# Kernel tuning notes

Hardware: AMD Instinct MI355X
Metric: run time of the kernel (lower is better)

The kernel has to match this reference:

```python
import jax, jax.numpy as jnp
import numpy as np

B, NPTS, T, P, C, D = 2, 32768, 32768, 512, 4, 768


def _sincos_pos_embed(centers, embed_dim):
    # centers: np [P,3]; matches get_3d_sincos_pos_embed
    c = centers - centers.mean(axis=0)
    c = c / np.linalg.norm(c, axis=1).max()
    div = np.exp(np.arange(0, embed_dim, 6) * -(np.log(10000.0) / embed_dim))  # [D/6]
    arg = c[:, None, :] * div[None, :, None]                                   # [P, D/6, 3]
    pe = np.concatenate([np.sin(arg), np.cos(arg)], axis=-1).reshape(centers.shape[0], embed_dim)
    return pe.astype(np.float32)


def setup_inputs() -> dict:
    key = jax.random.key(0)
    ks = jax.random.split(key, 12)
    rng = np.random.default_rng(0)

    # ragged patch sizes (avg 64) summing exactly to T
    sizes = rng.integers(32, 97, size=P).astype(np.int64)
    sizes = np.maximum((sizes * (T / sizes.sum())).astype(np.int64), 1)
    sizes[-1] += T - sizes.sum()
    patch_offset = jnp.asarray(np.concatenate([[0], np.cumsum(sizes)]), dtype=jnp.int32)  # [P+1]

    patch_index = jax.random.randint(ks[0], (T,), 0, NPTS, dtype=jnp.int32)
    latent = jax.random.normal(ks[1], (B, NPTS, C), dtype=jnp.float32)

    s = 0.02
    params = dict(
        w1a=jax.random.normal(ks[2], (C, D), jnp.float32) * s,
        b1a=jnp.zeros((D,), jnp.float32),
        w1b=jax.random.normal(ks[3], (D, D), jnp.float32) * s,
        b1b=jnp.zeros((D,), jnp.float32),
        w2a=jax.random.normal(ks[4], (2 * D, D), jnp.float32) * s,
        b2a=jnp.zeros((D,), jnp.float32),
        g2=jnp.ones((D,), jnp.float32),
        beta2=jnp.zeros((D,), jnp.float32),
        w2b=jax.random.normal(ks[5], (D, D), jnp.float32) * s,
        b2b=jnp.zeros((D,), jnp.float32),
    )

    centers = rng.standard_normal((P, 3))
    pos_embed = jnp.asarray(_sincos_pos_embed(centers, D))[None]  # [1, P, D]

    return dict(latent=latent, patch_index=patch_index, patch_offset=patch_offset,
                pos_embed=pos_embed, **params)


def _ln(x, eps, gamma=None, beta=None):
    mu = x.mean(axis=-1, keepdims=True)
    var = ((x - mu) ** 2).mean(axis=-1, keepdims=True)
    y = (x - mu) * jax.lax.rsqrt(var + eps)
    if gamma is not None:
        y = y * gamma + beta
    return y


def reference(latent, patch_index, patch_offset, pos_embed,
              w1a, b1a, w1b, b1b, w2a, b2a, g2, beta2, w2b, b2b):
    T_ = patch_index.shape[0]
    P_ = patch_offset.shape[0] - 1
    # segment id of each token (repeat_interleave inverse): seg[t] = patch containing t
    seg = jnp.searchsorted(patch_offset[1:], jnp.arange(T_, dtype=patch_offset.dtype), side='right')

    x = latent[:, patch_index, :]                           # [B, T, C] gather
    h = x @ w1a + b1a
    h = jax.nn.gelu(_ln(h, 1e-6), approximate=False)
    h = h @ w1b + b1b                                       # [B, T, D]

    segmax = lambda a: jax.ops.segment_max(a, seg, num_segments=P_)
    y = jax.vmap(segmax)(h)                                 # [B, P, D] ragged max-pool

    h2 = jnp.concatenate([y[:, seg, :], h], axis=-1)        # repeat_interleave + concat
    h2 = h2 @ w2a + b2a
    h2 = jax.nn.gelu(_ln(h2, 1e-5, g2, beta2), approximate=False)
    h2 = h2 @ w2b + b2b                                     # [B, T, D]
    raw_latent = h2

    out = jax.vmap(segmax)(raw_latent) + pos_embed          # [B, P, D]
    return out.astype(raw_latent.dtype), raw_latent
```

## Files before the change

kernel.cpp:

```cpp
#include <hip/hip_runtime.h>
#include <hip/hip_bf16.h>
#include <math.h>

#define B_    2
#define NPTS_ 32768
#define T_    32768
#define P_    512
#define C_    4
#define D_    768
#define M_    (B_ * T_)

typedef __bf16 bf16_t;
typedef __bf16 bf16x8 __attribute__((ext_vector_type(8)));
typedef __bf16 bf16x4 __attribute__((ext_vector_type(4)));
typedef float  f32x4  __attribute__((ext_vector_type(4)));

__device__ inline void gload16(const void* g, void* l) {
  __builtin_amdgcn_global_load_lds(
      (const __attribute__((address_space(1))) void*)g,
      (__attribute__((address_space(3))) void*)l, 16, 0, 0);
}

__device__ inline float gelu_exact(float x) {
  return 0.5f * x * (1.0f + erff(x * 0.70710678118654752f));
}

__device__ inline unsigned fmap(float x) {
  unsigned u = __float_as_uint(x);
  return (u & 0x80000000u) ? ~u : (u | 0x80000000u);
}
__device__ inline float funmap(unsigned u) {
  unsigned v = (u & 0x80000000u) ? (u & 0x7FFFFFFFu) : ~u;
  return __uint_as_float(v);
}

__global__ void seg_kernel(const int* __restrict__ off, int* __restrict__ seg) {
  int t = blockIdx.x * blockDim.x + threadIdx.x;
  if (t >= T_) return;
  int lo = 0, hi = P_;
  while (lo < hi) {
    int mid = (lo + hi) >> 1;
    if (off[mid + 1] <= t) lo = mid + 1; else hi = mid;
  }
  seg[t] = lo;
}

__global__ __launch_bounds__(256) void init_umax_kernel(uint4* __restrict__ u) {
  u[blockIdx.x * 256 + threadIdx.x] = make_uint4(0, 0, 0, 0);
}

__global__ __launch_bounds__(256) void yconv_kernel(
    const uint4* __restrict__ ymax, bf16_t* __restrict__ y) {
  int t = blockIdx.x * 256 + threadIdx.x;
  uint4 u = ymax[t];
  bf16x4 o;
  o[0] = (bf16_t)funmap(u.x); o[1] = (bf16_t)funmap(u.y);
  o[2] = (bf16_t)funmap(u.z); o[3] = (bf16_t)funmap(u.w);
  *(bf16x4*)(y + (size_t)t * 4) = o;
}

__global__ __launch_bounds__(256) void final2_kernel(
    const uint4* __restrict__ rmax, const float4* __restrict__ pe,
    float4* __restrict__ out) {
  int t = blockIdx.x * 256 + threadIdx.x;
  int row = t / 192, col = t % 192;
  uint4 u = rmax[t];
  float4 p = pe[(row & (P_ - 1)) * 192 + col];
  float4 o;
  o.x = funmap(u.x) + p.x; o.y = funmap(u.y) + p.y;
  o.z = funmap(u.z) + p.z; o.w = funmap(u.w) + p.w;
  out[t] = o;
}

__global__ __launch_bounds__(256) void wconvT_kernel(
    const float* __restrict__ src, bf16_t* __restrict__ dst, int K, int N) {
  __shared__ float tile[32][33];
  int n0 = blockIdx.x * 32, k0 = blockIdx.y * 32;
  int tx = threadIdx.x, ty = threadIdx.y;
  #pragma unroll
  for (int i = 0; i < 4; ++i)
    tile[ty + 8 * i][tx] = src[(size_t)(k0 + ty + 8 * i) * N + n0 + tx];
  __syncthreads();
  #pragma unroll
  for (int i = 0; i < 4; ++i)
    dst[(size_t)(n0 + ty + 8 * i) * K + k0 + tx] = (bf16_t)tile[tx][ty + 8 * i];
}

__global__ __launch_bounds__(256) void embed_kernel(
    const float4* __restrict__ latent4, const int* __restrict__ pidx,
    const float* __restrict__ w1a, const float* __restrict__ b1a,
    bf16_t* __restrict__ act1) {
  int wid = threadIdx.x >> 6, lane = threadIdx.x & 63;
  int m = blockIdx.x * 4 + wid;
  int b = m >> 15, t = m & (T_ - 1);
  float4 x = latent4[(size_t)b * NPTS_ + pidx[t]];
  int d8 = lane * 8, d4 = 512 + lane * 4;
  float v[12];
  {
    float4 a0 = *(const float4*)(b1a + d8);
    float4 a1 = *(const float4*)(b1a + d8 + 4);
    float4 a2 = *(const float4*)(b1a + d4);
    v[0]=a0.x; v[1]=a0.y; v[2]=a0.z; v[3]=a0.w;
    v[4]=a1.x; v[5]=a1.y; v[6]=a1.z; v[7]=a1.w;
    v[8]=a2.x; v[9]=a2.y; v[10]=a2.z; v[11]=a2.w;
  }
  float xk[4] = {x.x, x.y, x.z, x.w};
  #pragma unroll
  for (int k = 0; k < 4; ++k) {
    const float* w = w1a + k * D_;
    float4 w0 = *(const float4*)(w + d8);
    float4 w1 = *(const float4*)(w + d8 + 4);
    float4 w2 = *(const float4*)(w + d4);
    float f = xk[k];
    v[0] += f*w0.x; v[1] += f*w0.y; v[2] += f*w0.z; v[3] += f*w0.w;
    v[4] += f*w1.x; v[5] += f*w1.y; v[6] += f*w1.z; v[7] += f*w1.w;
    v[8] += f*w2.x; v[9] += f*w2.y; v[10]+= f*w2.z; v[11]+= f*w2.w;
  }
  float sum = 0.f, sq = 0.f;
  #pragma unroll
  for (int j = 0; j < 12; ++j) { sum += v[j]; sq += v[j]*v[j]; }
  #pragma unroll
  for (int o = 32; o > 0; o >>= 1) { sum += __shfl_xor(sum, o); sq += __shfl_xor(sq, o); }
  float mu = sum * (1.0f / D_);
  float rstd = rsqrtf(sq * (1.0f / D_) - mu * mu + 1e-6f);
  bf16x8 o8; bf16x4 o4;
  #pragma unroll
  for (int j = 0; j < 8; ++j) o8[j] = (bf16_t)gelu_exact((v[j] - mu) * rstd);
  #pragma unroll
  for (int j = 0; j < 4; ++j) o4[j] = (bf16_t)gelu_exact((v[8 + j] - mu) * rstd);
  size_t base = (size_t)m * D_;
  *(bf16x8*)(act1 + base + d8) = o8;
  *(bf16x4*)(act1 + base + d4) = o4;
}

__global__ __launch_bounds__(256) void ln2_kernel(
    const bf16_t* __restrict__ h2pre, const float* __restrict__ z,
    const int* __restrict__ seg, const float* __restrict__ g2,
    const float* __restrict__ beta2, bf16_t* __restrict__ act2) {
  int wid = threadIdx.x >> 6, lane = threadIdx.x & 63;
  int m = blockIdx.x * 4 + wid;
  int b = m >> 15, t = m & (T_ - 1);
  int d8 = lane * 8, d4 = 512 + lane * 4;
  size_t base = (size_t)m * D_;
  const float* zrow = z + (size_t)((b << 9) + seg[t]) * D_;
  bf16x8 i8 = *(const bf16x8*)(h2pre + base + d8);
  bf16x4 i4 = *(const bf16x4*)(h2pre + base + d4);
  float4 z0 = *(const float4*)(zrow + d8);
  float4 z1 = *(const float4*)(zrow + d8 + 4);
  float4 z2 = *(const float4*)(zrow + d4);
  float v[12];
  #pragma unroll
  for (int j = 0; j < 8; ++j) v[j] = (float)i8[j];
  #pragma unroll
  for (int j = 0; j < 4; ++j) v[8 + j] = (float)i4[j];
  v[0]+=z0.x; v[1]+=z0.y; v[2]+=z0.z; v[3]+=z0.w;
  v[4]+=z1.x; v[5]+=z1.y; v[6]+=z1.z; v[7]+=z1.w;
  v[8]+=z2.x; v[9]+=z2.y; v[10]+=z2.z; v[11]+=z2.w;
  float sum = 0.f, sq = 0.f;
  #pragma unroll
  for (int j = 0; j < 12; ++j) { sum += v[j]; sq += v[j]*v[j]; }
  #pragma unroll
  for (int o = 32; o > 0; o >>= 1) { sum += __shfl_xor(sum, o); sq += __shfl_xor(sq, o); }
  float mu = sum * (1.0f / D_);
  float rstd = rsqrtf(sq * (1.0f / D_) - mu * mu + 1e-5f);
  float4 ga = *(const float4*)(g2 + d8);
  float4 gb = *(const float4*)(g2 + d8 + 4);
  float4 gc = *(const float4*)(g2 + d4);
  float4 ba = *(const float4*)(beta2 + d8);
  float4 bb = *(const float4*)(beta2 + d8 + 4);
  float4 bc = *(const float4*)(beta2 + d4);
  float g[12] = {ga.x,ga.y,ga.z,ga.w, gb.x,gb.y,gb.z,gb.w, gc.x,gc.y,gc.z,gc.w};
  float be[12]= {ba.x,ba.y,ba.z,ba.w, bb.x,bb.y,bb.z,bb.w, bc.x,bc.y,bc.z,bc.w};
  bf16x8 o8; bf16x4 o4;
  #pragma unroll
  for (int j = 0; j < 8; ++j) o8[j] = (bf16_t)gelu_exact((v[j] - mu) * rstd * g[j] + be[j]);
  #pragma unroll
  for (int j = 0; j < 4; ++j) o4[j] = (bf16_t)gelu_exact((v[8+j] - mu) * rstd * g[8+j] + be[8+j]);
  *(bf16x8*)(act2 + base + d8) = o8;
  *(bf16x4*)(act2 + base + d4) = o4;
}

template <int MODE, bool SEGMAX, typename OutT>
__global__ __launch_bounds__(256) void gemm_kernel(
    const bf16_t* __restrict__ A, const bf16_t* __restrict__ BT,
    const float* __restrict__ addend, OutT* __restrict__ C,
    int M, int N, int K, const int* __restrict__ seg,
    unsigned* __restrict__ gmax) {
  __shared__ bf16_t As[128 * 32];
  __shared__ bf16_t Bs[128 * 32];
  __shared__ int segm[128];
  int tid = threadIdx.x;
  int wave = tid >> 6, lane = tid & 63;
  int lr = lane & 15, hi = lane >> 4;
  int wm = wave >> 1, wn = wave & 1;

  int nb = gridDim.x * gridDim.y;
  int bid = blockIdx.y * gridDim.x + blockIdx.x;
  int per = nb >> 3;
  int w = (bid & 7) * per + (bid >> 3);
  int wx = w % gridDim.x, wy = w / gridDim.x;
  int n0 = wx * 128, m0 = wy * 128;

  if (SEGMAX) {
    if (tid < 128) segm[tid] = seg[(m0 + tid) & (T_ - 1)];
  }

  f32x4 acc[4][4] = {};

  for (int kt = 0; kt < K; kt += 32) {
    __syncthreads();
    #pragma unroll
    for (int q = 0; q < 2; ++q) {
      int c = q * 256 + tid;
      int row = c >> 2, ko = (c & 3) * 8;
      gload16(A + (size_t)(m0 + row) * K + (kt + ko), (char*)As + q * 4096 + wave * 1024);
      gload16(BT + (size_t)(n0 + row) * K + (kt + ko), (char*)Bs + q * 4096 + wave * 1024);
    }
    __syncthreads();

    bf16x8 af[4], bfr[4];
    #pragma unroll
    for (int i = 0; i < 4; ++i)
      af[i] = *reinterpret_cast<const bf16x8*>(&As[(size_t)(wm * 64 + i * 16 + lr) * 32 + hi * 8]);
    #pragma unroll
    for (int j = 0; j < 4; ++j)
      bfr[j] = *reinterpret_cast<const bf16x8*>(&Bs[(size_t)(wn * 64 + j * 16 + lr) * 32 + hi * 8]);
    #pragma unroll
    for (int i = 0; i < 4; ++i)
      #pragma unroll
      for (int j = 0; j < 4; ++j)
        acc[i][j] = __builtin_amdgcn_mfma_f32_16x16x32_bf16(af[i], bfr[j], acc[i][j], 0, 0, 0);
  }

  unsigned* smax = reinterpret_cast<unsigned*>(As);
  int sb = 0, zb = 0;
  if (SEGMAX) {
    __syncthreads();
    for (int q = tid; q < 8 * 128; q += 256) smax[q] = 0u;
    sb = segm[0];
    zb = (m0 >> 15) << 9;
    __syncthreads();
  }

  #pragma unroll
  for (int j = 0; j < 4; ++j) {
    int nl = wn * 64 + j * 16 + lr;
    int n = n0 + nl;
    float bv = (MODE == 0) ? addend[n] : 0.f;
    #pragma unroll
    for (int i = 0; i < 4; ++i) {
      int rbase = wm * 64 + i * 16 + hi * 4;
      float vv[4];
      #pragma unroll
      for (int r = 0; r < 4; ++r) {
        vv[r] = acc[i][j][r] + bv;
        C[(size_t)(m0 + rbase + r) * N + n] = (OutT)vv[r];
      }
      if (SEGMAX) {
        int sA = segm[rbase] - sb, sB = segm[rbase + 3] - sb;
        if (sA == sB) {
          float mx = fmaxf(fmaxf(vv[0], vv[1]), fmaxf(vv[2], vv[3]));
          atomicMax(&smax[sA * 128 + nl], fmap(mx));
        } else {
          #pragma unroll
          for (int r = 0; r < 4; ++r)
            atomicMax(&smax[(segm[rbase + r] - sb) * 128 + nl], fmap(vv[r]));
        }
      }
    }
  }

  if (SEGMAX) {
    __syncthreads();
    int nseg = segm[127] - sb + 1;
    for (int q = tid; q < nseg * 128; q += 256) {
      int sl = q >> 7, nl2 = q & 127;
      atomicMax(&gmax[(size_t)(zb + sb + sl) * D_ + n0 + nl2], smax[q]);
    }
  }
}

extern "C" void kernel_launch(void* const* d_in, const int* in_sizes, int n_in,
                              void* d_out, int out_size, void* d_ws, size_t ws_size,
                              hipStream_t stream) {
  const float* latent       = (const float*)d_in[0];
  const int*   patch_index  = (const int*)d_in[1];
  const int*   patch_offset = (const int*)d_in[2];
  const float* pos_embed    = (const float*)d_in[3];
  const float* w1a  = (const float*)d_in[4];
  const float* b1a  = (const float*)d_in[5];
  const float* w1b  = (const float*)d_in[6];
  const float* b1b  = (const float*)d_in[7];
  const float* w2a  = (const float*)d_in[8];
  const float* b2a  = (const float*)d_in[9];
  const float* g2   = (const float*)d_in[10];
  const float* beta2= (const float*)d_in[11];
  const float* w2b  = (const float*)d_in[12];
  const float* b2b  = (const float*)d_in[13];

  float* out_f   = (float*)d_out;
  float* raw_out = out_f + (size_t)B_ * P_ * D_;

  char* ws = (char*)d_ws;
  size_t off = 0;
  auto take = [&](size_t bytes) {
    off = (off + 255) & ~(size_t)255;
    char* p = ws + off;
    off += bytes;
    return p;
  };
  int*      seg   = (int*)     take((size_t)T_ * 4);
  bf16_t*   w1bT  = (bf16_t*)  take((size_t)D_ * D_ * 2);
  bf16_t*   w2aTT = (bf16_t*)  take((size_t)D_ * D_ * 2);
  bf16_t*   w2aBT = (bf16_t*)  take((size_t)D_ * D_ * 2);
  bf16_t*   w2bT  = (bf16_t*)  take((size_t)D_ * D_ * 2);
  bf16_t*   ybuf  = (bf16_t*)  take((size_t)B_ * P_ * D_ * 2);
  float*    zbuf  = (float*)   take((size_t)B_ * P_ * D_ * 4);
  unsigned* umax  = (unsigned*)take((size_t)2 * B_ * P_ * D_ * 4);
  unsigned* ymax  = umax;
  unsigned* rmax  = umax + (size_t)B_ * P_ * D_;
  bf16_t*   bufY  = (bf16_t*)  take((size_t)M_ * D_ * 2);
  size_t needX = (size_t)M_ * D_ * 2;
  size_t offX  = (off + 255) & ~(size_t)255;
  bf16_t* bufX;
  if (offX + needX <= ws_size) {
    bufX = (bf16_t*)take(needX);
  } else {
    bufX = (bf16_t*)raw_out;
  }

  seg_kernel<<<(T_ + 255) / 256, 256, 0, stream>>>(patch_offset, seg);
  init_umax_kernel<<<(2 * B_ * P_ * D_) / (4 * 256), 256, 0, stream>>>((uint4*)umax);
  dim3 wcb(32, 8);
  wconvT_kernel<<<dim3(D_/32, D_/32), wcb, 0, stream>>>(w1b, w1bT, D_, D_);
  wconvT_kernel<<<dim3(D_/32, D_/32), wcb, 0, stream>>>(w2a, w2aTT, D_, D_);
  wconvT_kernel<<<dim3(D_/32, D_/32), wcb, 0, stream>>>(w2a + (size_t)D_*D_, w2aBT, D_, D_);
  wconvT_kernel<<<dim3(D_/32, D_/32), wcb, 0, stream>>>(w2b, w2bT, D_, D_);

  embed_kernel<<<M_ / 4, 256, 0, stream>>>((const float4*)latent, patch_index, w1a, b1a, bufX);

  gemm_kernel<0, true, bf16_t><<<dim3(D_/128, M_/128), 256, 0, stream>>>(
      bufX, w1bT, b1b, bufY, M_, D_, D_, seg, ymax);

  yconv_kernel<<<(B_ * P_ * D_) / (4 * 256), 256, 0, stream>>>((const uint4*)ymax, ybuf);

  gemm_kernel<0, false, float><<<dim3(D_/128, (B_*P_)/128), 256, 0, stream>>>(
      ybuf, w2aTT, b2a, zbuf, B_*P_, D_, D_, nullptr, nullptr);

  gemm_kernel<1, false, bf16_t><<<dim3(D_/128, M_/128), 256, 0, stream>>>(
      bufY, w2aBT, nullptr, bufX, M_, D_, D_, nullptr, nullptr);

  ln2_kernel<<<M_ / 4, 256, 0, stream>>>(bufX, zbuf, seg, g2, beta2, bufY);

  gemm_kernel<0, true, float><<<dim3(D_/128, M_/128), 256, 0, stream>>>(
      bufY, w2bT, b2b, raw_out, M_, D_, D_, seg, rmax);

  final2_kernel<<<(B_ * P_ * D_) / (4 * 256), 256, 0, stream>>>(
      (const uint4*)rmax, (const float4*)pos_embed, (float4*)out_f);
}
```

Measured before the change: 535.5 us.

## Replace 128x128 GEMM with double-buffered 256x256 tile kernel using swizzled LDS

Replaces the simple 128x128, K=32 single-buffered GEMM with a 256x256-tile, 512-thread kernel. It uses K=64 steps, two LDS stages (128KB) filled by async global-to-LDS loads, and an XOR-swizzled LDS layout to avoid bank conflicts. The main loop interleaves fragment loads, prefetch of the next stage and MFMA bursts with setprio and barriers, aiming to hide memory latency and raise MFMA utilisation. The small GEMM over 1024 rows now launches only 12 blocks, and the large LDS footprint limits each CU to one block.

Result: faster. 456.9 us (-14.7%).

```diff
diff --git a/kernel.cpp b/kernel.cpp
--- a/kernel.cpp
+++ b/kernel.cpp
@@ -180,91 +180,182 @@
   *(bf16x4*)(act2 + base + d4) = o4;
 }
 
-template <int MODE, bool SEGMAX, typename OutT>
-__global__ __launch_bounds__(256) void gemm_kernel(
+#define STAGE_A(P2, KTG)                                                     \
+  { _Pragma("unroll")                                                        \
+    for (int h = 0; h < 2; ++h) {                                            \
+      _Pragma("unroll")                                                      \
+      for (int ps = 0; ps < 2; ++ps) {                                       \
+        int c = ps * 512 + wid * 64 + lane;                                  \
+        int rw = c >> 3;                                                     \
+        int cs = (c & 7) ^ (rw & 7);                                         \
+        gload16(A + (size_t)(m0 + h * 128 + rw) * 768 + (KTG) + cs * 8,      \
+                lds + (P2) * 65536 + h * 16384 + ps * 8192 + wid * 1024);    \
+      } } }
+
+#define STAGE_B(P2, KTG)                                                     \
+  { _Pragma("unroll")                                                        \
+    for (int h = 0; h < 2; ++h) {                                            \
+      _Pragma("unroll")                                                      \
+      for (int ps = 0; ps < 2; ++ps) {                                       \
+        int c = ps * 512 + wid * 64 + lane;                                  \
+        int rw = c >> 3;                                                     \
+        int cs = (c & 7) ^ (rw & 7);                                         \
+        gload16(BT + (size_t)(n0 + h * 128 + rw) * 768 + (KTG) + cs * 8,     \
+                lds + (P2) * 65536 + 32768 + h * 16384 + ps * 8192 + wid * 1024); \
+      } } }
+
+template <bool HASBIAS, bool SEGMAX, typename OutT>
+__global__ __launch_bounds__(512, 1) void gemm256_kernel(
     const bf16_t* __restrict__ A, const bf16_t* __restrict__ BT,
-    const float* __restrict__ addend, OutT* __restrict__ C,
-    int M, int N, int K, const int* __restrict__ seg,
-    unsigned* __restrict__ gmax) {
-  __shared__ bf16_t As[128 * 32];
-  __shared__ bf16_t Bs[128 * 32];
-  __shared__ int segm[128];
+    const float* __restrict__ bias, OutT* __restrict__ C,
+    const int* __restrict__ seg, unsigned* __restrict__ gmax) {
+  constexpr int NT = 12;
+  __shared__ __align__(16) char lds[131072];
+  __shared__ int segm[256];
   int tid = threadIdx.x;
-  int wave = tid >> 6, lane = tid & 63;
+  int wid = tid >> 6, lane = tid & 63;
   int lr = lane & 15, hi = lane >> 4;
-  int wm = wave >> 1, wn = wave & 1;
-
-  int nb = gridDim.x * gridDim.y;
-  int bid = blockIdx.y * gridDim.x + blockIdx.x;
-  int per = nb >> 3;
-  int w = (bid & 7) * per + (bid >> 3);
-  int wx = w % gridDim.x, wy = w / gridDim.x;
-  int n0 = wx * 128, m0 = wy * 128;
-
-  if (SEGMAX) {
-    if (tid < 128) segm[tid] = seg[(m0 + tid) & (T_ - 1)];
-  }
-
-  f32x4 acc[4][4] = {};
-
-  for (int kt = 0; kt < K; kt += 32) {
-    __syncthreads();
-    #pragma unroll
-    for (int q = 0; q < 2; ++q) {
-      int c = q * 256 + tid;
-      int row = c >> 2, ko = (c & 3) * 8;
-      gload16(A + (size_t)(m0 + row) * K + (kt + ko), (char*)As + q * 4096 + wave * 1024);
-      gload16(BT + (size_t)(n0 + row) * K + (kt + ko), (char*)Bs + q * 4096 + wave * 1024);
-    }
-    __syncthreads();
-
-    bf16x8 af[4], bfr[4];
-    #pragma unroll
-    for (int i = 0; i < 4; ++i)
-      af[i] = *reinterpret_cast<const bf16x8*>(&As[(size_t)(wm * 64 + i * 16 + lr) * 32 + hi * 8]);
-    #pragma unroll
-    for (int j = 0; j < 4; ++j)
-      bfr[j] = *reinterpret_cast<const bf16x8*>(&Bs[(size_t)(wn * 64 + j * 16 + lr) * 32 + hi * 8]);
-    #pragma unroll
-    for (int i = 0; i < 4; ++i)
-      #pragma unroll
-      for (int j = 0; j < 4; ++j)
-        acc[i][j] = __builtin_amdgcn_mfma_f32_16x16x32_bf16(af[i], bfr[j], acc[i][j], 0, 0, 0);
-  }
-
-  unsigned* smax = reinterpret_cast<unsigned*>(As);
+  int wm = wid >> 2, wn = wid & 3;
+
+  int gx = gridDim.x;
+  int nb = gx * gridDim.y;
+  int bid = blockIdx.y * gx + blockIdx.x;
+  int w = ((nb & 7) == 0) ? ((bid & 7) * (nb >> 3) + (bid >> 3)) : bid;
+  int bx = w % gx, by = w / gx;
+  int n0 = bx * 256, m0 = by * 256;
+
+  if (SEGMAX) { if (tid < 256) segm[tid] = seg[(m0 + tid) & (T_ - 1)]; }
+
+  f32x4 acc[8][4] = {};
+  bf16x8 af0[4][2], af1[4][2], bf0[2][2], bf1[2][2];
+  int cx = lr & 7;
+
+  STAGE_A(0, 0); STAGE_B(0, 0);
+  STAGE_A(1, 64); STAGE_B(1, 64);
+
+  for (int j = 0; j < NT; ++j) {
+    int p = j & 1;
+    const char* base = lds + p * 65536;
+    if (j < NT - 1) asm volatile("s_waitcnt vmcnt(8)" ::: "memory");
+    else            asm volatile("s_waitcnt vmcnt(0)" ::: "memory");
+    __builtin_amdgcn_s_barrier();
+    #pragma unroll
+    for (int i = 0; i < 4; ++i)
+      #pragma unroll
+      for (int s = 0; s < 2; ++s) {
+        int row = i * 16 + lr;
+        int ch = (s * 4 + hi) ^ cx;
+        af0[i][s] = *(const bf16x8*)(base + wm * 16384 + row * 128 + ch * 16);
+      }
+    #pragma unroll
+    for (int jb = 0; jb < 2; ++jb)
+      #pragma unroll
+      for (int s = 0; s < 2; ++s) {
+        int nrow = wn * 64 + jb * 16 + lr;
+        int ch = (s * 4 + hi) ^ cx;
+        bf0[jb][s] = *(const bf16x8*)(base + 32768 + (nrow >> 7) * 16384 +
+                                      (nrow & 127) * 128 + ch * 16);
+      }
+    __builtin_amdgcn_s_barrier();
+    __builtin_amdgcn_s_setprio(1);
+    #pragma unroll
+    for (int i = 0; i < 4; ++i)
+      #pragma unroll
+      for (int jb = 0; jb < 2; ++jb)
+        #pragma unroll
+        for (int s = 0; s < 2; ++s)
+          acc[i][jb] = __builtin_amdgcn_mfma_f32_16x16x32_bf16(af0[i][s], bf0[jb][s], acc[i][jb], 0, 0, 0);
+    __builtin_amdgcn_s_setprio(0);
+    __builtin_amdgcn_s_barrier();
+
+    #pragma unroll
+    for (int i = 0; i < 4; ++i)
+      #pragma unroll
+      for (int s = 0; s < 2; ++s) {
+        int row = 64 + i * 16 + lr;
+        int ch = (s * 4 + hi) ^ cx;
+        af1[i][s] = *(const bf16x8*)(base + wm * 16384 + row * 128 + ch * 16);
+      }
+    __builtin_amdgcn_s_barrier();
+    __builtin_amdgcn_s_setprio(1);
+    #pragma unroll
+    for (int i = 0; i < 4; ++i)
+      #pragma unroll
+      for (int jb = 0; jb < 2; ++jb)
+        #pragma unroll
+        for (int s = 0; s < 2; ++s)
+          acc[4 + i][jb] = __builtin_amdgcn_mfma_f32_16x16x32_bf16(af1[i][s], bf0[jb][s], acc[4 + i][jb], 0, 0, 0);
+    __builtin_amdgcn_s_setprio(0);
+    __builtin_amdgcn_s_barrier();
+
+    #pragma unroll
+    for (int jb = 0; jb < 2; ++jb)
+      #pragma unroll
+      for (int s = 0; s < 2; ++s) {
+        int nrow = wn * 64 + 32 + jb * 16 + lr;
+        int ch = (s * 4 + hi) ^ cx;
+        bf1[jb][s] = *(const bf16x8*)(base + 32768 + (nrow >> 7) * 16384 +
+                                      (nrow & 127) * 128 + ch * 16);
+      }
+    if (j + 2 < NT) STAGE_A(p, (j + 2) * 64);
+    __builtin_amdgcn_s_barrier();
+    __builtin_amdgcn_s_setprio(1);
+    #pragma unroll
+    for (int i = 0; i < 4; ++i)
+      #pragma unroll
+      for (int jb = 0; jb < 2; ++jb)
+        #pragma unroll
+        for (int s = 0; s < 2; ++s)
+          acc[i][2 + jb] = __builtin_amdgcn_mfma_f32_16x16x32_bf16(af0[i][s], bf1[jb][s], acc[i][2 + jb], 0, 0, 0);
+    __builtin_amdgcn_s_setprio(0);
+    __builtin_amdgcn_s_barrier();
+
+    if (j + 2 < NT) STAGE_B(p, (j + 2) * 64);
+    __builtin_amdgcn_s_barrier();
+    __builtin_amdgcn_s_setprio(1);
+    #pragma unroll
+    for (int i = 0; i < 4; ++i)
+      #pragma unroll
+      for (int jb = 0; jb < 2; ++jb)
+        #pragma unroll
+        for (int s = 0; s < 2; ++s)
+          acc[4 + i][2 + jb] = __builtin_amdgcn_mfma_f32_16x16x32_bf16(af1[i][s], bf1[jb][s], acc[4 + i][2 + jb], 0, 0, 0);
+    __builtin_amdgcn_s_setprio(0);
+  }
+
+  unsigned* smax = reinterpret_cast<unsigned*>(lds);
   int sb = 0, zb = 0;
   if (SEGMAX) {
-    __syncthreads();
-    for (int q = tid; q < 8 * 128; q += 256) smax[q] = 0u;
+    __builtin_amdgcn_s_barrier();
     sb = segm[0];
     zb = (m0 >> 15) << 9;
+    for (int q = tid; q < 16 * 256; q += 512) smax[q] = 0u;
     __syncthreads();
   }
 
   #pragma unroll
-  for (int j = 0; j < 4; ++j) {
-    int nl = wn * 64 + j * 16 + lr;
+  for (int jn = 0; jn < 4; ++jn) {
+    int nl = wn * 64 + jn * 16 + lr;
     int n = n0 + nl;
-    float bv = (MODE == 0) ? addend[n] : 0.f;
-    #pragma unroll
-    for (int i = 0; i < 4; ++i) {
-      int rbase = wm * 64 + i * 16 + hi * 4;
+    float bv = HASBIAS ? bias[n] : 0.f;
+    #pragma unroll
+    for (int i = 0; i < 8; ++i) {
+      int rb = wm * 128 + i * 16 + hi * 4;
       float vv[4];
       #pragma unroll
       for (int r = 0; r < 4; ++r) {
-        vv[r] = acc[i][j][r] + bv;
-        C[(size_t)(m0 + rbase + r) * N + n] = (OutT)vv[r];
+        vv[r] = acc[i][jn][r] + bv;
+        C[(size_t)(m0 + rb + r) * 768 + n] = (OutT)vv[r];
       }
       if (SEGMAX) {
-        int sA = segm[rbase] - sb, sB = segm[rbase + 3] - sb;
+        int sA = segm[rb] - sb, sB = segm[rb + 3] - sb;
         if (sA == sB) {
           float mx = fmaxf(fmaxf(vv[0], vv[1]), fmaxf(vv[2], vv[3]));
-          atomicMax(&smax[sA * 128 + nl], fmap(mx));
+          atomicMax(&smax[sA * 256 + nl], fmap(mx));
         } else {
           #pragma unroll
           for (int r = 0; r < 4; ++r)
-            atomicMax(&smax[(segm[rbase + r] - sb) * 128 + nl], fmap(vv[r]));
+            atomicMax(&smax[(segm[rb + r] - sb) * 256 + nl], fmap(vv[r]));
         }
       }
     }
@@ -272,10 +363,10 @@
 
   if (SEGMAX) {
     __syncthreads();
-    int nseg = segm[127] - sb + 1;
-    for (int q = tid; q < nseg * 128; q += 256) {
-      int sl = q >> 7, nl2 = q & 127;
-      atomicMax(&gmax[(size_t)(zb + sb + sl) * D_ + n0 + nl2], smax[q]);
+    int nseg = segm[255] - sb + 1;
+    for (int q = tid; q < nseg * 256; q += 512) {
+      int sl = q >> 8, nl2 = q & 255;
+      atomicMax(&gmax[(size_t)(zb + sb + sl) * 768 + n0 + nl2], smax[q]);
     }
   }
 }
@@ -339,21 +430,21 @@
 
   embed_kernel<<<M_ / 4, 256, 0, stream>>>((const float4*)latent, patch_index, w1a, b1a, bufX);
 
-  gemm_kernel<0, true, bf16_t><<<dim3(D_/128, M_/128), 256, 0, stream>>>(
-      bufX, w1bT, b1b, bufY, M_, D_, D_, seg, ymax);
+  gemm256_kernel<true, true, bf16_t><<<dim3(3, M_/256), 512, 0, stream>>>(
+      bufX, w1bT, b1b, bufY, seg, ymax);
 
   yconv_kernel<<<(B_ * P_ * D_) / (4 * 256), 256, 0, stream>>>((const uint4*)ymax, ybuf);
 
-  gemm_kernel<0, false, float><<<dim3(D_/128, (B_*P_)/128), 256, 0, stream>>>(
-      ybuf, w2aTT, b2a, zbuf, B_*P_, D_, D_, nullptr, nullptr);
-
-  gemm_kernel<1, false, bf16_t><<<dim3(D_/128, M_/128), 256, 0, stream>>>(
-      bufY, w2aBT, nullptr, bufX, M_, D_, D_, nullptr, nullptr);
+  gemm256_kernel<true, false, float><<<dim3(3, (B_*P_)/256), 512, 0, stream>>>(
+      ybuf, w2aTT, b2a, zbuf, nullptr, nullptr);
+
+  gemm256_kernel<false, false, bf16_t><<<dim3(3, M_/256), 512, 0, stream>>>(
+      bufY, w2aBT, nullptr, bufX, nullptr, nullptr);
 
   ln2_kernel<<<M_ / 4, 256, 0, stream>>>(bufX, zbuf, seg, g2, beta2, bufY);
 
-  gemm_kernel<0, true, float><<<dim3(D_/128, M_/128), 256, 0, stream>>>(
-      bufY, w2bT, b2b, raw_out, M_, D_, D_, seg, rmax);
+  gemm256_kernel<true, true, float><<<dim3(3, M_/256), 512, 0, stream>>>(
+      bufY, w2bT, b2b, raw_out, seg, rmax);
 
   final2_kernel<<<(B_ * P_ * D_) / (4 * 256), 256, 0, stream>>>(
       (const uint4*)rmax, (const float4*)pos_embed, (float4*)out_f);
```
